# Optimization experiments

Measured on AMD Instinct MI355X. Metric: run time of the kernel, lower is better.

The kernel has to match this reference:

```python
import jax, jax.numpy as jnp
import numpy as np

BATCH, SEQ, HIDDEN = 2, 4096, 4096
HEADS, HEAD_DIM, BLOCK = 32, 128, 256
LAYER_IDX, N_LAYERS = 1, 32
EPS = 1e-5


def setup_inputs() -> dict:
    key = jax.random.key(0)
    ks = jax.random.split(key, 5)
    s = 0.02
    return {
        "hidden_states": jax.random.normal(ks[0], (BATCH, SEQ, HIDDEN), jnp.float32),
        "qkv_w": jax.random.normal(ks[1], (3 * HEADS * HEAD_DIM, HIDDEN), jnp.float32) * s,
        "out_w": jax.random.normal(ks[2], (HIDDEN, HEADS * HEAD_DIM), jnp.float32) * s,
        "gate_w": jax.random.normal(ks[3], (HEADS * HEAD_DIM, HIDDEN), jnp.float32) * s,
        "norm_w": jnp.ones((HEADS * HEAD_DIM,), jnp.float32),
    }


def _decays():
    # slope_rate: (h,1,1)
    base = 1.0 / 2.0 ** (8.0 / HEADS)
    exponent = jnp.arange(HEADS, dtype=jnp.float32) + 1.0
    factor = 1.0 - LAYER_IDX / (N_LAYERS - 1 + 1e-5) + 1e-5
    slope = (base ** exponent * factor)[:, None, None]
    r = jnp.arange(BLOCK, dtype=jnp.float32) + 1.0
    q_decay = jnp.exp(-slope * r[:, None])                 # (h, block, 1)
    k_decay = jnp.exp(-slope * (BLOCK - r)[:, None])       # (h, block, 1)
    diff = r[:, None] - r[None, :]                         # (block, block): i - j
    diag = slope[None] * diff[None, None]                  # (1, h, block, block)
    diag = jnp.where(diag >= 0, -diag, -jnp.inf)
    diag_decay = jnp.exp(diag)                             # causal intra-block decay
    block_decay = jnp.exp(-slope * BLOCK)                  # (h,1,1)
    return q_decay, k_decay, diag_decay, block_decay


def reference(hidden_states, qkv_w, out_w, gate_w, norm_w):
    b, s, _ = hidden_states.shape
    h, d, bs = HEADS, HEAD_DIM, BLOCK
    nb = s // bs
    q_decay, k_decay, diag_decay, block_decay = _decays()

    # qkv projection + silu, split per-head into q,k,v
    qkv = jax.nn.silu(hidden_states @ qkv_w.T)             # (b,s,3hd)
    qkv = qkv.reshape(b, s, h, 3, d)
    q = jnp.moveaxis(qkv[:, :, :, 0], 2, 1)                # (b,h,s,d)
    k = jnp.moveaxis(qkv[:, :, :, 1], 2, 1)
    v = jnp.moveaxis(qkv[:, :, :, 2], 2, 1)

    # split sequence into blocks, scan leading axis = block index
    def to_blocks(x):
        return jnp.moveaxis(x.reshape(b, h, nb, bs, d), 2, 0)  # (nb,b,h,bs,d)

    qb, kb, vb = to_blocks(q), to_blocks(k), to_blocks(v)

    def step(kv, blk):
        cq, ck, cv = blk
        # intra-block quadratic attention with causal decay
        scores = jnp.einsum('bhnd,bhmd->bhnm', cq, ck) * diag_decay
        intra = jnp.einsum('bhnm,bhmd->bhnd', scores, cv)
        # inter-block via decayed recurrent state kv: (b,h,d,d)
        inter = jnp.einsum('bhnd,bhde->bhne', cq * q_decay, kv)
        kv_next = kv * block_decay + jnp.einsum('bhnd,bhne->bhde', ck * k_decay, cv)
        return kv_next, intra + inter

    kv0 = jnp.zeros((b, h, d, d), hidden_states.dtype)
    _, out_blocks = jax.lax.scan(step, kv0, (qb, kb, vb))  # (nb,b,h,bs,d)

    attn = jnp.moveaxis(out_blocks, 0, 2)                  # (b,h,nb,bs,d)
    attn = attn.reshape(b, h, s, d).transpose(0, 2, 1, 3).reshape(b, s, h * d)

    # RMSNorm (fp32 accumulation, as MixtralRMSNorm)
    xf = attn.astype(jnp.float32)
    xf = xf * jax.lax.rsqrt(jnp.mean(xf * xf, axis=-1, keepdims=True) + EPS)
    normed = norm_w * xf.astype(attn.dtype)

    gate = jax.nn.sigmoid(hidden_states @ gate_w.T)
    return (gate * normed) @ out_w.T
```

## Files before the change

kernel.cpp:

```cpp
#include <hip/hip_runtime.h>

typedef unsigned short u16;
typedef __attribute__((ext_vector_type(4))) float f32x4;
typedef __attribute__((ext_vector_type(8))) __bf16 bf16x8;

#define SEQ   4096
#define HID   4096
#define HID3  12288

__device__ __forceinline__ float bf2f(u16 u){
  union { unsigned int i; float f; } v; v.i = ((unsigned int)u) << 16; return v.f;
}
__device__ __forceinline__ u16 f2bf(float f){
  union { float f; unsigned int i; } v; v.f = f;
  unsigned int r = (v.i + 0x7FFFu + ((v.i >> 16) & 1u)) >> 16;
  return (u16)r;
}
__device__ __forceinline__ float slope_of(int h){
  const float factor = 1.0f - 1.0f/(31.0f + 1e-5f) + 1e-5f;
  return exp2f(-0.25f * (float)(h + 1)) * factor;
}
__device__ __forceinline__ bf16x8 ld_bf8(const u16* p){
  return __builtin_bit_cast(bf16x8, *(const uint4*)p);
}
__device__ __forceinline__ void gload_lds16(const u16* g, u16* l){
  __builtin_amdgcn_global_load_lds((const __attribute__((address_space(1))) void*)g,
                                   (__attribute__((address_space(3))) void*)l, 16, 0, 0);
}

__global__ __launch_bounds__(256) void cvt_kernel(const float* __restrict__ in,
                                                  u16* __restrict__ out, long n){
  long i = ((long)blockIdx.x * 256 + threadIdx.x) * 4;
  long stride = (long)gridDim.x * 1024;
  for (; i < n; i += stride){
    float4 v = *(const float4*)(in + i);
    ushort4 o;
    o.x = f2bf(v.x); o.y = f2bf(v.y); o.z = f2bf(v.z); o.w = f2bf(v.w);
    *(ushort4*)(out + i) = o;
  }
}

template<int EPI>
__global__ __launch_bounds__(512) void gemm256(
    const u16* __restrict__ A, const u16* __restrict__ B, void* __restrict__ C,
    const u16* __restrict__ Aux, int M, int N, int K)
{
  __shared__ u16 ring[5][16384];
  const int t = threadIdx.x;
  const int w = t >> 6, l = t & 63, lr = l & 15, lk = l >> 4;
  const int mw = w >> 2, nw = w & 3;
  const int nbn = N >> 8;
  int nwg = gridDim.x;
  int bid = blockIdx.x;
  int bswz = (bid & 7) * (nwg >> 3) + (bid >> 3);
  int bm = bswz / nbn, bn = bswz % nbn;
  const u16* Abase = A + (long)(bm * 256) * K;
  const u16* Bbase = B + (long)(bn * 256) * K;
  const int NT = K >> 6;

  int sr[2], sku[2];
#pragma unroll
  for (int i = 0; i < 2; ++i){
    int dr = i * 64 + (t >> 3);
    int ul = (t & 7) ^ (dr & 7);
    sr[i]  = 2 * dr + (ul >> 2);
    sku[i] = ul & 3;
  }
  int offA[8], offB[4];
#pragma unroll
  for (int fn = 0; fn < 8; ++fn){
    int row = mw * 128 + fn * 16 + lr;
    offA[fn] = (row >> 1) * 64 + (((((row & 1) << 2) + lk) ^ ((row >> 1) & 7)) << 3);
  }
#pragma unroll
  for (int fe = 0; fe < 4; ++fe){
    int row = nw * 64 + fe * 16 + lr;
    offB[fe] = (row >> 1) * 64 + (((((row & 1) << 2) + lk) ^ ((row >> 1) & 7)) << 3);
  }

  auto stageA = [&](int kt, int c, int slot, int i){
    gload_lds16(Abase + (long)sr[i] * K + kt * 64 + c * 32 + sku[i] * 8,
                &ring[slot][i * 4096 + w * 512]);
  };
  auto stageB = [&](int kt, int c, int slot, int i){
    gload_lds16(Bbase + (long)sr[i] * K + kt * 64 + c * 32 + sku[i] * 8,
                &ring[slot][8192 + i * 4096 + w * 512]);
  };

  f32x4 acc[8][4] = {};

  stageA(0,0,0,0); stageA(0,0,0,1); stageB(0,0,0,0); stageB(0,0,0,1);
  stageA(0,1,1,0); stageA(0,1,1,1); stageB(0,1,1,0); stageB(0,1,1,1);
  if (1 < NT){ stageA(1,0,2,0); stageA(1,0,2,1); stageB(1,0,2,0); stageB(1,0,2,1); }
  asm volatile("s_waitcnt vmcnt(4)" ::: "memory");
  __builtin_amdgcn_s_barrier();

  int sa = 0;
  for (int p = 0; p < NT; ++p){
    int sb = sa + 1; if (sb >= 5) sb -= 5;
    int sx = sa + 3; if (sx >= 5) sx -= 5;
    int sy = sa + 4; if (sy >= 5) sy -= 5;
    const u16* Aa = &ring[sa][0];
    const u16* Ab = &ring[sb][0];
    const u16* Ba = &ring[sa][8192];
    const u16* Bb = &ring[sb][8192];
    bf16x8 bh[4][2], af[4][2][2];
#pragma unroll
    for (int q = 0; q < 4; ++q){
      if (q == 0){
#pragma unroll
        for (int fe = 0; fe < 4; ++fe){
          bh[fe][0] = ld_bf8(Ba + offB[fe]);
          bh[fe][1] = ld_bf8(Bb + offB[fe]);
        }
#pragma unroll
        for (int fnl = 0; fnl < 2; ++fnl){
          af[0][fnl][0] = ld_bf8(Aa + offA[fnl]);
          af[0][fnl][1] = ld_bf8(Ab + offA[fnl]);
        }
#pragma unroll
        for (int fnl = 0; fnl < 2; ++fnl){
          af[1][fnl][0] = ld_bf8(Aa + offA[2 + fnl]);
          af[1][fnl][1] = ld_bf8(Ab + offA[2 + fnl]);
        }
        if (p + 1 < NT){ stageA(p+1, 1, sx, 0); stageA(p+1, 1, sx, 1); }
      } else if (q == 1){
#pragma unroll
        for (int fnl = 0; fnl < 2; ++fnl){
          af[2][fnl][0] = ld_bf8(Aa + offA[4 + fnl]);
          af[2][fnl][1] = ld_bf8(Ab + offA[4 + fnl]);
        }
        if (p + 1 < NT){ stageB(p+1, 1, sx, 0); stageB(p+1, 1, sx, 1); }
      } else if (q == 2){
#pragma unroll
        for (int fnl = 0; fnl < 2; ++fnl){
          af[3][fnl][0] = ld_bf8(Aa + offA[6 + fnl]);
          af[3][fnl][1] = ld_bf8(Ab + offA[6 + fnl]);
        }
        if (p + 2 < NT){ stageA(p+2, 0, sy, 0); stageA(p+2, 0, sy, 1); }
      } else {
        if (p + 2 < NT){ stageB(p+2, 0, sy, 0); stageB(p+2, 0, sy, 1); }
      }
      if (q < 3) asm volatile("s_waitcnt lgkmcnt(4)" ::: "memory");
      else       asm volatile("s_waitcnt lgkmcnt(0)" ::: "memory");
      __builtin_amdgcn_sched_barrier(0);
      __builtin_amdgcn_s_setprio(1);
#pragma unroll
      for (int fnl = 0; fnl < 2; ++fnl)
#pragma unroll
        for (int fe = 0; fe < 4; ++fe){
          acc[q*2+fnl][fe] = __builtin_amdgcn_mfma_f32_16x16x32_bf16(af[q][fnl][0], bh[fe][0], acc[q*2+fnl][fe], 0, 0, 0);
          acc[q*2+fnl][fe] = __builtin_amdgcn_mfma_f32_16x16x32_bf16(af[q][fnl][1], bh[fe][1], acc[q*2+fnl][fe], 0, 0, 0);
        }
      __builtin_amdgcn_s_setprio(0);
    }
    if (p + 2 < NT) asm volatile("s_waitcnt vmcnt(4)" ::: "memory");
    else            asm volatile("s_waitcnt vmcnt(0)" ::: "memory");
    __builtin_amdgcn_s_barrier();
    sa += 2; if (sa >= 5) sa -= 5;
  }

  long crow = (long)bm * 256 + mw * 128 + lk * 4;
  long ccol = (long)bn * 256 + nw * 64 + lr;
#pragma unroll
  for (int fn = 0; fn < 8; ++fn)
#pragma unroll
    for (int fe = 0; fe < 4; ++fe)
#pragma unroll
      for (int reg = 0; reg < 4; ++reg){
        long row = crow + fn * 16 + reg;
        long col = ccol + fe * 16;
        float x = acc[fn][fe][reg];
        if (EPI == 0){
          ((u16*)C)[row * N + col] = f2bf(x / (1.0f + __expf(-x)));
        } else if (EPI == 1){
          float g = 1.0f / (1.0f + __expf(-x));
          ((u16*)C)[row * N + col] = f2bf(g * bf2f(Aux[row * N + col]));
        } else {
          ((float*)C)[row * N + col] = x;
        }
      }
}

__global__ __launch_bounds__(256) void attn_contrib(
    const u16* __restrict__ qkv, float* __restrict__ ct)
{
  __shared__ u16 kb[256 * 128];
  __shared__ u16 vb[256 * 128];
  __shared__ float kdec[256];
  int wg = blockIdx.x;
  int bh = wg >> 4, blk = wg & 15;
  int b = bh >> 5, h = bh & 31;
  int t = threadIdx.x;
  float slope = slope_of(h);
  kdec[t] = __expf(-slope * (float)(255 - t));
  const u16* kg = qkv + ((long)(b * SEQ + blk * 256)) * HID3 + h * 384 + 128;
  const u16* vg = kg + 128;
#pragma unroll
  for (int i = 0; i < 16; ++i){
    int chunk = t + i * 256;
    int row = chunk >> 4, c8 = (chunk & 15) << 3;
    *(uint4*)&kb[row * 128 + c8] = *(const uint4*)&kg[(long)row * HID3 + c8];
    *(uint4*)&vb[row * 128 + c8] = *(const uint4*)&vg[(long)row * HID3 + c8];
  }
  __syncthreads();
  int e0 = (t >> 4) << 3, d0 = (t & 15) << 3;
  float acc[8][8];
#pragma unroll
  for (int i = 0; i < 8; ++i)
#pragma unroll
    for (int j = 0; j < 8; ++j) acc[i][j] = 0.f;
  for (int n = 0; n < 256; ++n){
    float kd = kdec[n];
    uint4 vv = *(const uint4*)&vb[n * 128 + e0];
    uint4 kk = *(const uint4*)&kb[n * 128 + d0];
    const u16* vs = (const u16*)&vv;
    const u16* ks = (const u16*)&kk;
    float ve[8], kf[8];
#pragma unroll
    for (int x = 0; x < 8; ++x){ ve[x] = bf2f(vs[x]); kf[x] = bf2f(ks[x]) * kd; }
#pragma unroll
    for (int i = 0; i < 8; ++i)
#pragma unroll
      for (int j = 0; j < 8; ++j) acc[i][j] += ve[i] * kf[j];
  }
  float* out = ct + (long)wg * 16384;
#pragma unroll
  for (int i = 0; i < 8; ++i){
    *(float4*)&out[(e0 + i) * 128 + d0]     = make_float4(acc[i][0], acc[i][1], acc[i][2], acc[i][3]);
    *(float4*)&out[(e0 + i) * 128 + d0 + 4] = make_float4(acc[i][4], acc[i][5], acc[i][6], acc[i][7]);
  }
}

__global__ __launch_bounds__(256) void attn_scan(const float* __restrict__ ct,
                                                 u16* __restrict__ stTb)
{
  int g = blockIdx.x;
  int bh = g >> 2, sl = g & 3;
  int t = threadIdx.x;
  float bdec = __expf(-slope_of(bh & 31) * 256.0f);
  float cur[16];
#pragma unroll
  for (int i = 0; i < 16; ++i) cur[i] = 0.f;
  const float* base = ct + (long)bh * 16 * 16384 + sl * 4096;
  u16* ob = stTb + (long)bh * 16 * 16384 + sl * 4096;
  for (int blkI = 0; blkI < 16; ++blkI){
    const float* p = base + (long)blkI * 16384;
    u16* o = ob + (long)blkI * 16384;
#pragma unroll
    for (int i = 0; i < 16; ++i){
      o[t + i * 256] = f2bf(cur[i]);
      cur[i] = cur[i] * bdec + p[t + i * 256];
    }
  }
}

__global__ __launch_bounds__(512) void attn_mfma(
    const u16* __restrict__ qkv, const u16* __restrict__ stTb, u16* __restrict__ attn)
{
  __shared__ u16 Ks[256 * 130];
  __shared__ u16 VTs[128 * 258];
  __shared__ u16 Ps[4][64 * 34];
  int wg = blockIdx.x;
  int bh = wg >> 4, blk = wg & 15;
  int b = bh >> 5, h = bh & 31;
  int t = threadIdx.x;
  int w = t >> 6, l = t & 63, lr = l & 15, lk = l >> 4;
  int r = w >> 1, c = w & 1;
  float slope = slope_of(h);
  const u16* qg = qkv + ((long)(b * SEQ + blk * 256)) * HID3 + h * 384;
  const u16* kg = qg + 128;
  const u16* vg = qg + 256;

#pragma unroll
  for (int i = 0; i < 8; ++i){
    int chunk = t + i * 512;
    int row = chunk >> 4, c8 = (chunk & 15) << 3;
    *(uint4*)&Ks[row * 130 + c8] = *(const uint4*)&kg[(long)row * HID3 + c8];
    uint4 vv = *(const uint4*)&vg[(long)row * HID3 + c8];
    const u16* vs = (const u16*)&vv;
#pragma unroll
    for (int x = 0; x < 8; ++x) VTs[(c8 + x) * 258 + row] = vs[x];
  }
  bf16x8 qa[4][4];
#pragma unroll
  for (int fn = 0; fn < 4; ++fn)
#pragma unroll
    for (int kc = 0; kc < 4; ++kc)
      qa[fn][kc] = ld_bf8(&qg[(long)(r * 64 + fn * 16 + lr) * HID3 + kc * 32 + lk * 8]);
  f32x4 acc[4][4] = {};
  __syncthreads();

  int mtmax = 2 * r + 1;
  for (int mt = 0; mt < 8; ++mt){
    if (mt <= mtmax){
      f32x4 S[4] = {};
      int mrow = mt * 32 + c * 16 + lr;
      bf16x8 kb[4];
#pragma unroll
      for (int kc = 0; kc < 4; ++kc)
        kb[kc] = ld_bf8(&Ks[mrow * 130 + kc * 32 + lk * 8]);
#pragma unroll
      for (int fn = 0; fn < 4; ++fn)
#pragma unroll
        for (int kc = 0; kc < 4; ++kc)
          S[fn] = __builtin_amdgcn_mfma_f32_16x16x32_bf16(qa[fn][kc], kb[kc], S[fn], 0, 0, 0);
      int m = mt * 32 + c * 16 + lr;
#pragma unroll
      for (int fn = 0; fn < 4; ++fn)
#pragma unroll
        for (int reg = 0; reg < 4; ++reg){
          int n = r * 64 + fn * 16 + lk * 4 + reg;
          float dv = (n >= m) ? __expf(-slope * (float)(n - m)) : 0.f;
          Ps[r][(fn * 16 + lk * 4 + reg) * 34 + c * 16 + lr] = f2bf(S[fn][reg] * dv);
        }
    }
    __syncthreads();
    if (mt <= mtmax){
      bf16x8 pa[4], vb[4];
#pragma unroll
      for (int fn = 0; fn < 4; ++fn)
        pa[fn] = ld_bf8(&Ps[r][(fn * 16 + lr) * 34 + lk * 8]);
#pragma unroll
      for (int fe = 0; fe < 4; ++fe)
        vb[fe] = ld_bf8(&VTs[(c * 64 + fe * 16 + lr) * 258 + mt * 32 + lk * 8]);
#pragma unroll
      for (int fn = 0; fn < 4; ++fn)
#pragma unroll
        for (int fe = 0; fe < 4; ++fe)
          acc[fn][fe] = __builtin_amdgcn_mfma_f32_16x16x32_bf16(pa[fn], vb[fe], acc[fn][fe], 0, 0, 0);
    }
    __syncthreads();
  }

#pragma unroll
  for (int fn = 0; fn < 4; ++fn){
    int n = r * 64 + fn * 16 + lr;
    float qd = __expf(-slope * (float)(n + 1));
#pragma unroll
    for (int kc = 0; kc < 4; ++kc){
      union { bf16x8 v; u16 u[8]; } uu; uu.v = qa[fn][kc];
#pragma unroll
      for (int x = 0; x < 8; ++x) uu.u[x] = f2bf(bf2f(uu.u[x]) * qd);
      qa[fn][kc] = uu.v;
    }
  }
  const u16* sg = stTb + (long)(bh * 16 + blk) * 16384;
#pragma unroll
  for (int kc = 0; kc < 4; ++kc){
    bf16x8 sb2[4];
#pragma unroll
    for (int fe = 0; fe < 4; ++fe)
      sb2[fe] = ld_bf8(&sg[(c * 64 + fe * 16 + lr) * 128 + kc * 32 + lk * 8]);
#pragma unroll
    for (int fn = 0; fn < 4; ++fn)
#pragma unroll
      for (int fe = 0; fe < 4; ++fe)
        acc[fn][fe] = __builtin_amdgcn_mfma_f32_16x16x32_bf16(qa[fn][kc], sb2[fe], acc[fn][fe], 0, 0, 0);
  }

  u16* arow = attn + ((long)(b * SEQ + blk * 256)) * HID + h * 128;
#pragma unroll
  for (int fn = 0; fn < 4; ++fn)
#pragma unroll
    for (int fe = 0; fe < 4; ++fe)
#pragma unroll
      for (int reg = 0; reg < 4; ++reg){
        int n = r * 64 + fn * 16 + lk * 4 + reg;
        int col = c * 64 + fe * 16 + lr;
        arow[(long)n * HID + col] = f2bf(acc[fn][fe][reg]);
      }
}

__global__ __launch_bounds__(256) void rmsnorm_ip(u16* __restrict__ attn,
                                                  const float* __restrict__ nw)
{
  __shared__ float wsum[4];
  int row = blockIdx.x, t = threadIdx.x;
  u16* p = attn + (long)row * HID;
  uint4 v0 = *(const uint4*)&p[t * 8];
  uint4 v1 = *(const uint4*)&p[t * 8 + 2048];
  const u16* a0 = (const u16*)&v0;
  const u16* a1 = (const u16*)&v1;
  float f0[8], f1[8];
  float ss = 0.f;
#pragma unroll
  for (int x = 0; x < 8; ++x){
    f0[x] = bf2f(a0[x]); f1[x] = bf2f(a1[x]);
    ss += f0[x] * f0[x] + f1[x] * f1[x];
  }
#pragma unroll
  for (int off = 32; off > 0; off >>= 1) ss += __shfl_down(ss, off);
  if ((t & 63) == 0) wsum[t >> 6] = ss;
  __syncthreads();
  float rs = rsqrtf((wsum[0] + wsum[1] + wsum[2] + wsum[3]) * (1.0f / 4096.0f) + 1e-5f);
  alignas(16) u16 o0[8], o1[8];
#pragma unroll
  for (int x = 0; x < 8; ++x){
    o0[x] = f2bf(f0[x] * rs * nw[t * 8 + x]);
    o1[x] = f2bf(f1[x] * rs * nw[t * 8 + 2048 + x]);
  }
  *(uint4*)&p[t * 8]        = *(const uint4*)&o0[0];
  *(uint4*)&p[t * 8 + 2048] = *(const uint4*)&o1[0];
}

extern "C" void kernel_launch(void* const* d_in, const int* in_sizes, int n_in,
                              void* d_out, int out_size, void* d_ws, size_t ws_size,
                              hipStream_t stream)
{
  const float* hidden = (const float*)d_in[0];
  const float* qkv_w  = (const float*)d_in[1];
  const float* out_w  = (const float*)d_in[2];
  const float* gate_w = (const float*)d_in[3];
  const float* norm_w = (const float*)d_in[4];
  char* ws = (char*)d_ws;
  const long SZ_X  = 67108864L;
  const long SZ_WQ = 100663296L;
  const long SZ_WG = 33554432L;
  const long SZ_WO = 33554432L;
  const long SZ_QA = 201326592L;
  const long SZ_AT = 67108864L;
  u16* Xb   = (u16*)(ws);
  u16* Wq   = (u16*)(ws + SZ_X);
  u16* Wg   = (u16*)(ws + SZ_X + SZ_WQ);
  u16* Wo   = (u16*)(ws + SZ_X + SZ_WQ + SZ_WG);
  u16* qact = (u16*)(ws + SZ_X + SZ_WQ + SZ_WG + SZ_WO);
  u16* attn = (u16*)(ws + SZ_X + SZ_WQ + SZ_WG + SZ_WO + SZ_QA);
  float* st   = (float*)Wq;
  u16*   stTb = (u16*)(ws + SZ_X + 67108864L);
  u16* gated = qact;
  if (ws_size < (size_t)(SZ_X + SZ_WQ + SZ_WG + SZ_WO + SZ_QA + SZ_AT)) return;

  cvt_kernel<<<1024, 256, 0, stream>>>(hidden, Xb, 33554432L);
  cvt_kernel<<<1024, 256, 0, stream>>>(qkv_w,  Wq, 50331648L);
  cvt_kernel<<<1024, 256, 0, stream>>>(gate_w, Wg, 16777216L);
  cvt_kernel<<<1024, 256, 0, stream>>>(out_w,  Wo, 16777216L);

  gemm256<0><<<32 * 48, 512, 0, stream>>>(Xb, Wq, (void*)qact, nullptr, 8192, 12288, 4096);

  attn_contrib<<<1024, 256, 0, stream>>>(qact, st);
  attn_scan<<<256, 256, 0, stream>>>(st, stTb);
  attn_mfma<<<1024, 512, 0, stream>>>(qact, stTb, attn);
  rmsnorm_ip<<<8192, 256, 0, stream>>>(attn, norm_w);

  gemm256<1><<<32 * 16, 512, 0, stream>>>(Xb, Wg, (void*)gated, attn, 8192, 4096, 4096);
  gemm256<2><<<32 * 16, 512, 0, stream>>>(gated, Wo, d_out, nullptr, 8192, 4096, 4096);
}
```

Before: 1.699 ms.

## Use 32x32 MFMA in GEMM and move attention contribution onto MFMA

The GEMM switches from 16x16x32 to 32x32x16 bf16 MFMA tiles, with new LDS fragment offsets and an epilogue remapped to the 32x32 accumulator layout. The intended gain is fewer LDS fragment loads per MFMA and fewer instructions. Separately, the per-block K^T V contribution kernel replaces its scalar FP32 outer-product loop with MFMA. To do this it transposes K (pre-scaled by its decay) and V into padded LDS tiles. The cost is that the decayed K is rounded to bf16 before accumulation, and the transposed LDS writes are scattered.

```diff
diff --git a/kernel.cpp b/kernel.cpp
--- a/kernel.cpp
+++ b/kernel.cpp
@@ -2,6 +2,7 @@
 
 typedef unsigned short u16;
 typedef __attribute__((ext_vector_type(4))) float f32x4;
+typedef __attribute__((ext_vector_type(16))) float f32x16;
 typedef __attribute__((ext_vector_type(8))) __bf16 bf16x8;
 
 #define SEQ   4096
@@ -47,7 +48,8 @@
 {
   __shared__ u16 ring[5][16384];
   const int t = threadIdx.x;
-  const int w = t >> 6, l = t & 63, lr = l & 15, lk = l >> 4;
+  const int w = t >> 6, l = t & 63;
+  const int lr32 = l & 31, lk5 = l >> 5;
   const int mw = w >> 2, nw = w & 3;
   const int nbn = N >> 8;
   int nwg = gridDim.x;
@@ -66,17 +68,23 @@
     sr[i]  = 2 * dr + (ul >> 2);
     sku[i] = ul & 3;
   }
-  int offA[8], offB[4];
-#pragma unroll
-  for (int fn = 0; fn < 8; ++fn){
-    int row = mw * 128 + fn * 16 + lr;
-    offA[fn] = (row >> 1) * 64 + (((((row & 1) << 2) + lk) ^ ((row >> 1) & 7)) << 3);
-  }
-#pragma unroll
-  for (int fe = 0; fe < 4; ++fe){
-    int row = nw * 64 + fe * 16 + lr;
-    offB[fe] = (row >> 1) * 64 + (((((row & 1) << 2) + lk) ^ ((row >> 1) & 7)) << 3);
-  }
+  int offA[4][2], offB[2][2];
+#pragma unroll
+  for (int mt = 0; mt < 4; ++mt)
+#pragma unroll
+    for (int kcl = 0; kcl < 2; ++kcl){
+      int row = mw * 128 + mt * 32 + lr32;
+      int k8 = kcl * 2 + lk5;
+      offA[mt][kcl] = (row >> 1) * 64 + (((((row & 1) << 2) + k8) ^ ((row >> 1) & 7)) << 3);
+    }
+#pragma unroll
+  for (int nt = 0; nt < 2; ++nt)
+#pragma unroll
+    for (int kcl = 0; kcl < 2; ++kcl){
+      int row = nw * 64 + nt * 32 + lr32;
+      int k8 = kcl * 2 + lk5;
+      offB[nt][kcl] = (row >> 1) * 64 + (((((row & 1) << 2) + k8) ^ ((row >> 1) & 7)) << 3);
+    }
 
   auto stageA = [&](int kt, int c, int slot, int i){
     gload_lds16(Abase + (long)sr[i] * K + kt * 64 + c * 32 + sku[i] * 8,
@@ -87,7 +95,7 @@
                 &ring[slot][8192 + i * 4096 + w * 512]);
   };
 
-  f32x4 acc[8][4] = {};
+  f32x16 acc[4][2] = {};
 
   stageA(0,0,0,0); stageA(0,0,0,1); stageB(0,0,0,0); stageB(0,0,0,1);
   stageA(0,1,1,0); stageA(0,1,1,1); stageB(0,1,1,0); stageB(0,1,1,1);
@@ -104,38 +112,40 @@
     const u16* Ab = &ring[sb][0];
     const u16* Ba = &ring[sa][8192];
     const u16* Bb = &ring[sb][8192];
-    bf16x8 bh[4][2], af[4][2][2];
+    bf16x8 bh[2][4], af[4][4];
 #pragma unroll
     for (int q = 0; q < 4; ++q){
       if (q == 0){
 #pragma unroll
-        for (int fe = 0; fe < 4; ++fe){
-          bh[fe][0] = ld_bf8(Ba + offB[fe]);
-          bh[fe][1] = ld_bf8(Bb + offB[fe]);
-        }
-#pragma unroll
-        for (int fnl = 0; fnl < 2; ++fnl){
-          af[0][fnl][0] = ld_bf8(Aa + offA[fnl]);
-          af[0][fnl][1] = ld_bf8(Ab + offA[fnl]);
-        }
-#pragma unroll
-        for (int fnl = 0; fnl < 2; ++fnl){
-          af[1][fnl][0] = ld_bf8(Aa + offA[2 + fnl]);
-          af[1][fnl][1] = ld_bf8(Ab + offA[2 + fnl]);
+        for (int nt = 0; nt < 2; ++nt){
+          bh[nt][0] = ld_bf8(Ba + offB[nt][0]);
+          bh[nt][1] = ld_bf8(Ba + offB[nt][1]);
+          bh[nt][2] = ld_bf8(Bb + offB[nt][0]);
+          bh[nt][3] = ld_bf8(Bb + offB[nt][1]);
+        }
+#pragma unroll
+        for (int kc = 0; kc < 2; ++kc){
+          af[0][kc]     = ld_bf8(Aa + offA[0][kc]);
+          af[0][kc + 2] = ld_bf8(Ab + offA[0][kc]);
+        }
+#pragma unroll
+        for (int kc = 0; kc < 2; ++kc){
+          af[1][kc]     = ld_bf8(Aa + offA[1][kc]);
+          af[1][kc + 2] = ld_bf8(Ab + offA[1][kc]);
         }
         if (p + 1 < NT){ stageA(p+1, 1, sx, 0); stageA(p+1, 1, sx, 1); }
       } else if (q == 1){
 #pragma unroll
-        for (int fnl = 0; fnl < 2; ++fnl){
-          af[2][fnl][0] = ld_bf8(Aa + offA[4 + fnl]);
-          af[2][fnl][1] = ld_bf8(Ab + offA[4 + fnl]);
+        for (int kc = 0; kc < 2; ++kc){
+          af[2][kc]     = ld_bf8(Aa + offA[2][kc]);
+          af[2][kc + 2] = ld_bf8(Ab + offA[2][kc]);
         }
         if (p + 1 < NT){ stageB(p+1, 1, sx, 0); stageB(p+1, 1, sx, 1); }
       } else if (q == 2){
 #pragma unroll
-        for (int fnl = 0; fnl < 2; ++fnl){
-          af[3][fnl][0] = ld_bf8(Aa + offA[6 + fnl]);
-          af[3][fnl][1] = ld_bf8(Ab + offA[6 + fnl]);
+        for (int kc = 0; kc < 2; ++kc){
+          af[3][kc]     = ld_bf8(Aa + offA[3][kc]);
+          af[3][kc + 2] = ld_bf8(Ab + offA[3][kc]);
         }
         if (p + 2 < NT){ stageA(p+2, 0, sy, 0); stageA(p+2, 0, sy, 1); }
       } else {
@@ -146,12 +156,12 @@
       __builtin_amdgcn_sched_barrier(0);
       __builtin_amdgcn_s_setprio(1);
 #pragma unroll
-      for (int fnl = 0; fnl < 2; ++fnl)
-#pragma unroll
-        for (int fe = 0; fe < 4; ++fe){
-          acc[q*2+fnl][fe] = __builtin_amdgcn_mfma_f32_16x16x32_bf16(af[q][fnl][0], bh[fe][0], acc[q*2+fnl][fe], 0, 0, 0);
-          acc[q*2+fnl][fe] = __builtin_amdgcn_mfma_f32_16x16x32_bf16(af[q][fnl][1], bh[fe][1], acc[q*2+fnl][fe], 0, 0, 0);
-        }
+      for (int nt = 0; nt < 2; ++nt){
+        acc[q][nt] = __builtin_amdgcn_mfma_f32_32x32x16_bf16(af[q][0], bh[nt][0], acc[q][nt], 0, 0, 0);
+        acc[q][nt] = __builtin_amdgcn_mfma_f32_32x32x16_bf16(af[q][1], bh[nt][1], acc[q][nt], 0, 0, 0);
+        acc[q][nt] = __builtin_amdgcn_mfma_f32_32x32x16_bf16(af[q][2], bh[nt][2], acc[q][nt], 0, 0, 0);
+        acc[q][nt] = __builtin_amdgcn_mfma_f32_32x32x16_bf16(af[q][3], bh[nt][3], acc[q][nt], 0, 0, 0);
+      }
       __builtin_amdgcn_s_setprio(0);
     }
     if (p + 2 < NT) asm volatile("s_waitcnt vmcnt(4)" ::: "memory");
@@ -160,17 +170,17 @@
     sa += 2; if (sa >= 5) sa -= 5;
   }
 
-  long crow = (long)bm * 256 + mw * 128 + lk * 4;
-  long ccol = (long)bn * 256 + nw * 64 + lr;
-#pragma unroll
-  for (int fn = 0; fn < 8; ++fn)
-#pragma unroll
-    for (int fe = 0; fe < 4; ++fe)
-#pragma unroll
-      for (int reg = 0; reg < 4; ++reg){
-        long row = crow + fn * 16 + reg;
-        long col = ccol + fe * 16;
-        float x = acc[fn][fe][reg];
+  long crow = (long)bm * 256 + mw * 128 + 4 * lk5;
+  long ccol = (long)bn * 256 + nw * 64 + lr32;
+#pragma unroll
+  for (int mt = 0; mt < 4; ++mt)
+#pragma unroll
+    for (int nt = 0; nt < 2; ++nt)
+#pragma unroll
+      for (int reg = 0; reg < 16; ++reg){
+        long row = crow + mt * 32 + (reg & 3) + 8 * (reg >> 2);
+        long col = ccol + nt * 32;
+        float x = acc[mt][nt][reg];
         if (EPI == 0){
           ((u16*)C)[row * N + col] = f2bf(x / (1.0f + __expf(-x)));
         } else if (EPI == 1){
@@ -185,51 +195,57 @@
 __global__ __launch_bounds__(256) void attn_contrib(
     const u16* __restrict__ qkv, float* __restrict__ ct)
 {
-  __shared__ u16 kb[256 * 128];
-  __shared__ u16 vb[256 * 128];
-  __shared__ float kdec[256];
+  __shared__ u16 VT[128 * 258];
+  __shared__ u16 KT[128 * 258];
   int wg = blockIdx.x;
   int bh = wg >> 4, blk = wg & 15;
   int b = bh >> 5, h = bh & 31;
   int t = threadIdx.x;
   float slope = slope_of(h);
-  kdec[t] = __expf(-slope * (float)(255 - t));
   const u16* kg = qkv + ((long)(b * SEQ + blk * 256)) * HID3 + h * 384 + 128;
   const u16* vg = kg + 128;
 #pragma unroll
   for (int i = 0; i < 16; ++i){
     int chunk = t + i * 256;
     int row = chunk >> 4, c8 = (chunk & 15) << 3;
-    *(uint4*)&kb[row * 128 + c8] = *(const uint4*)&kg[(long)row * HID3 + c8];
-    *(uint4*)&vb[row * 128 + c8] = *(const uint4*)&vg[(long)row * HID3 + c8];
+    float kd = __expf(-slope * (float)(255 - row));
+    uint4 kk = *(const uint4*)&kg[(long)row * HID3 + c8];
+    uint4 vv = *(const uint4*)&vg[(long)row * HID3 + c8];
+    const u16* ks = (const u16*)&kk;
+    const u16* vs = (const u16*)&vv;
+#pragma unroll
+    for (int x = 0; x < 8; ++x){
+      KT[(c8 + x) * 258 + row] = f2bf(bf2f(ks[x]) * kd);
+      VT[(c8 + x) * 258 + row] = vs[x];
+    }
   }
   __syncthreads();
-  int e0 = (t >> 4) << 3, d0 = (t & 15) << 3;
-  float acc[8][8];
-#pragma unroll
-  for (int i = 0; i < 8; ++i)
-#pragma unroll
-    for (int j = 0; j < 8; ++j) acc[i][j] = 0.f;
-  for (int n = 0; n < 256; ++n){
-    float kd = kdec[n];
-    uint4 vv = *(const uint4*)&vb[n * 128 + e0];
-    uint4 kk = *(const uint4*)&kb[n * 128 + d0];
-    const u16* vs = (const u16*)&vv;
-    const u16* ks = (const u16*)&kk;
-    float ve[8], kf[8];
-#pragma unroll
-    for (int x = 0; x < 8; ++x){ ve[x] = bf2f(vs[x]); kf[x] = bf2f(ks[x]) * kd; }
-#pragma unroll
-    for (int i = 0; i < 8; ++i)
-#pragma unroll
-      for (int j = 0; j < 8; ++j) acc[i][j] += ve[i] * kf[j];
+  int w = t >> 6, l = t & 63, lr = l & 15, lk = l >> 4;
+  int we = (w >> 1) * 64, wd = (w & 1) * 64;
+  f32x4 acc[4][4] = {};
+  for (int nc = 0; nc < 8; ++nc){
+    bf16x8 va[4], kb[4];
+#pragma unroll
+    for (int f = 0; f < 4; ++f) va[f] = ld_bf8(&VT[(we + f * 16 + lr) * 258 + nc * 32 + lk * 8]);
+#pragma unroll
+    for (int f = 0; f < 4; ++f) kb[f] = ld_bf8(&KT[(wd + f * 16 + lr) * 258 + nc * 32 + lk * 8]);
+#pragma unroll
+    for (int fe = 0; fe < 4; ++fe)
+#pragma unroll
+      for (int fd = 0; fd < 4; ++fd)
+        acc[fe][fd] = __builtin_amdgcn_mfma_f32_16x16x32_bf16(va[fe], kb[fd], acc[fe][fd], 0, 0, 0);
   }
   float* out = ct + (long)wg * 16384;
 #pragma unroll
-  for (int i = 0; i < 8; ++i){
-    *(float4*)&out[(e0 + i) * 128 + d0]     = make_float4(acc[i][0], acc[i][1], acc[i][2], acc[i][3]);
-    *(float4*)&out[(e0 + i) * 128 + d0 + 4] = make_float4(acc[i][4], acc[i][5], acc[i][6], acc[i][7]);
-  }
+  for (int fe = 0; fe < 4; ++fe)
+#pragma unroll
+    for (int fd = 0; fd < 4; ++fd)
+#pragma unroll
+      for (int reg = 0; reg < 4; ++reg){
+        int e = we + fe * 16 + lk * 4 + reg;
+        int d = wd + fd * 16 + lr;
+        out[e * 128 + d] = acc[fe][fd][reg];
+      }
 }
 
 __global__ __launch_bounds__(256) void attn_scan(const float* __restrict__ ct,
```

Result: slower. 1.747 ms (+2.8%).
